# Kernel optimization log

Measured on AMD Instinct MI355X. Metric: run time of the kernel, lower is better.

Reference implementation:

```python
import jax, jax.numpy as jnp
import numpy as np

N_NODES = 100000
N_EDGES = 1600000
D_IN = 64
D_HID = 64


def setup_inputs() -> dict:
    key = jax.random.key(0)
    k1, k2, k3, k4, k5 = jax.random.split(key, 5)
    x = jax.random.normal(k1, (N_NODES, D_IN), dtype=jnp.float32)
    edge_index = jax.random.randint(k2, (2, N_EDGES), 0, N_NODES, dtype=jnp.int64)
    edge_weight = jax.random.uniform(k3, (N_EDGES,), dtype=jnp.float32)
    # GCNConv glorot-initialized linear weights (bias=False)
    s0 = (6.0 / (D_IN + D_HID)) ** 0.5
    W0 = jax.random.uniform(k4, (D_IN, D_HID), minval=-s0, maxval=s0, dtype=jnp.float32)
    s1 = (6.0 / (D_HID + D_HID)) ** 0.5
    W1 = jax.random.uniform(k5, (D_HID, D_HID), minval=-s1, maxval=s1, dtype=jnp.float32)
    return {"x": x, "edge_index": edge_index, "edge_weight": edge_weight, "W0": W0, "W1": W1}


def _gcn_layer(x, W, src, dst, edge_weight, deg_inv_sqrt, n_nodes):
    # h = X W  (bias=False)
    h = x @ W  # [N, D]
    # symmetric normalization including self-loops (weight 1)
    norm = deg_inv_sqrt[src] * edge_weight * deg_inv_sqrt[dst]  # [E]
    # gather src features, scale, scatter-sum at dst
    agg = jax.ops.segment_sum(norm[:, None] * h[src], dst, num_segments=n_nodes)
    # self-loop contribution: norm_ii = deg_inv_sqrt[i]^2 * 1
    agg = agg + (deg_inv_sqrt * deg_inv_sqrt)[:, None] * h
    return jax.nn.relu(agg)  # dropout is identity in eval mode


def reference(x, edge_index, edge_weight, W0, W1):
    src, dst = edge_index[0], edge_index[1]
    # degree with self-loops (self-loop weight = 1), aggregated at dst (source_to_target flow)
    deg = jax.ops.segment_sum(edge_weight, dst, num_segments=N_NODES) + 1.0
    deg_inv_sqrt = jax.lax.rsqrt(deg)
    x = _gcn_layer(x, W0, src, dst, edge_weight, deg_inv_sqrt, N_NODES)
    x = _gcn_layer(x, W1, src, dst, edge_weight, deg_inv_sqrt, N_NODES)
    return x
```

## Files before the change

### kernel.cpp

```cpp
#include <hip/hip_runtime.h>
#include <hip/hip_fp16.h>

#define D 64
#define BSH 9
#define BSZ (1 << BSH)
#define PB 2048
#define CAP 15360
#define SCAP 9216

__global__ __launch_bounds__(256) void initcur(int* __restrict__ ccur, int nbuck) {
    int t = threadIdx.x;
    if (t < nbuck) ccur[t] = t * CAP;
}

__global__ __launch_bounds__(512) void bucket1(const int* __restrict__ src,
                                               const int* __restrict__ dst,
                                               const float* __restrict__ ew,
                                               int* __restrict__ ccur,
                                               int2* __restrict__ pairs,
                                               int E, int nbuck) {
    __shared__ int hist[512];
    __shared__ int lbase[512];
    __shared__ int gbase[512];
    __shared__ int w0s[PB];
    __shared__ int w1s[PB];
    __shared__ unsigned short bids[PB];
    int t = threadIdx.x;
    hist[t] = 0;
    __syncthreads();
    int e0 = blockIdx.x * PB;
    int cnt = min(PB, E - e0);
    int b[4], lr[4], w0[4], w1[4];
    int i4 = t * 4;
    bool full4 = (i4 + 4 <= cnt);
    if (full4) {
        int4   s4 = *(const int4*)&src[e0 + i4];
        int4   d4 = *(const int4*)&dst[e0 + i4];
        float4 w4 = *(const float4*)&ew[e0 + i4];
        int ss[4] = {s4.x, s4.y, s4.z, s4.w};
        int ds[4] = {d4.x, d4.y, d4.z, d4.w};
        float wv[4] = {w4.x, w4.y, w4.z, w4.w};
#pragma unroll
        for (int k = 0; k < 4; ++k) {
            b[k]  = ds[k] >> BSH;
            w0[k] = ss[k] | ((ds[k] & (BSZ - 1)) << 17);
            w1[k] = __float_as_int(wv[k]);
            lr[k] = atomicAdd(&hist[b[k]], 1);
        }
    } else {
#pragma unroll
        for (int k = 0; k < 4; ++k) {
            int idx = i4 + k;
            if (idx < cnt) {
                int d = dst[e0 + idx];
                b[k]  = d >> BSH;
                w0[k] = src[e0 + idx] | ((d & (BSZ - 1)) << 17);
                w1[k] = __float_as_int(ew[e0 + idx]);
                lr[k] = atomicAdd(&hist[b[k]], 1);
            }
        }
    }
    __syncthreads();
    int hv = hist[t];
    lbase[t] = hv;
    __syncthreads();
    for (int off = 1; off < 512; off <<= 1) {
        int u = (t >= off) ? lbase[t - off] : 0;
        __syncthreads();
        lbase[t] += u;
        __syncthreads();
    }
    int excl = lbase[t] - hv;
    __syncthreads();
    lbase[t] = excl;
    if (t < nbuck && hv > 0) gbase[t] = atomicAdd(&ccur[t], hv);
    __syncthreads();
#pragma unroll
    for (int k = 0; k < 4; ++k) {
        int idx = i4 + k;
        if (idx < cnt) {
            int slot = lbase[b[k]] + lr[k];
            w0s[slot] = w0[k];
            w1s[slot] = w1[k];
            bids[slot] = (unsigned short)b[k];
        }
    }
    __syncthreads();
    for (int i = t; i < cnt; i += 512) {
        int bb = bids[i];
        int pos = gbase[bb] + (i - lbase[bb]);
        pairs[pos] = make_int2(w0s[i], w1s[i]);
    }
}

__global__ __launch_bounds__(512) void deg2(const int2* __restrict__ pairs,
                                            const int* __restrict__ ccur,
                                            int* __restrict__ offsets,
                                            int* __restrict__ ends,
                                            float* __restrict__ dis,
                                            int N, int nbuck) {
    __shared__ int cnt[512];
    __shared__ float sdeg[512];
    __shared__ int lb[512];
    int b = blockIdx.x;
    int t = threadIdx.x;
    cnt[t] = 0;
    sdeg[t] = 0.0f;
    __syncthreads();
    int base = b * CAP;
    int cntb = ccur[b] - base;
    for (int i = t; i < cntb; i += 512) {
        int2 p = pairs[base + i];
        int dl = p.x >> 17;
        atomicAdd(&cnt[dl], 1);
        atomicAdd(&sdeg[dl], __int_as_float(p.y));
    }
    __syncthreads();
    int node = (b << BSH) + t;
    int pc = (node < N) ? ((cnt[t] + 1 + 15) & ~15) : 0;
    lb[t] = pc;
    __syncthreads();
    for (int off = 1; off < 512; off <<= 1) {
        int u = (t >= off) ? lb[t - off] : 0;
        __syncthreads();
        lb[t] += u;
        __syncthreads();
    }
    int excl = lb[t] - pc;
    if (node < N) {
        offsets[node] = base + excl;
        ends[node]    = base + excl + pc;
        dis[node]     = rsqrtf(sdeg[t] + 1.0f);
    }
}

__global__ __launch_bounds__(512) void sort2b(int2* __restrict__ pairs,
                                              const int* __restrict__ ccur,
                                              const int* __restrict__ offsets,
                                              const int* __restrict__ ends,
                                              const float* __restrict__ dis,
                                              int N, int nbuck) {
    __shared__ int2 se[SCAP];
    __shared__ int cur[512];
    __shared__ float sdis[512];
    int b = blockIdx.x;
    int t = threadIdx.x;
    int base = b * CAP;
    int cntb = min(ccur[b] - base, SCAP);
    for (int i = t; i < cntb; i += 512) se[i] = pairs[base + i];
    int node = (b << BSH) + t;
    int end = 0; float dloc = 0.0f;
    if (node < N) {
        cur[t]  = offsets[node];
        end     = ends[node];
        dloc    = dis[node];
        sdis[t] = dloc;
    } else {
        cur[t] = 0; sdis[t] = 0.0f;
    }
    __syncthreads();
    for (int i = t; i < cntb; i += 512) {
        int2 p = se[i];
        int dl = p.x >> 17;
        int s  = p.x & 0x1FFFF;
        int pos = atomicAdd(&cur[dl], 1);
        float w = __int_as_float(p.y) * sdis[dl] * dis[s];
        pairs[pos] = make_int2(s, __float_as_int(w));
    }
    __syncthreads();
    if (node < N) {
        int c = cur[t];
        pairs[c] = make_int2(node, __float_as_int(dloc * dloc));
        for (int i = c + 1; i < end; ++i) pairs[i] = make_int2(0, 0);
    }
}

__global__ __launch_bounds__(256) void gemm64h(const float* __restrict__ X,
                                               const float* __restrict__ W,
                                               __half* __restrict__ Hb, int n) {
    __shared__ float Ws[64 * 64];
    __shared__ float Xs[16 * 64];
    for (int t = threadIdx.x; t < 64 * 64; t += 256) Ws[t] = W[t];
    int row0 = blockIdx.x * 16;
    for (int t = threadIdx.x; t < 16 * 64; t += 256) {
        int r = row0 + (t >> 6);
        Xs[t] = (r < n) ? X[r * 64 + (t & 63)] : 0.0f;
    }
    __syncthreads();
    int r  = threadIdx.x >> 4;
    int jc = (threadIdx.x & 15) * 4;
    float4 acc = make_float4(0.f, 0.f, 0.f, 0.f);
#pragma unroll
    for (int k = 0; k < 64; ++k) {
        float xv = Xs[r * 64 + k];
        float4 w = *(const float4*)&Ws[k * 64 + jc];
        acc.x += xv * w.x; acc.y += xv * w.y; acc.z += xv * w.z; acc.w += xv * w.w;
    }
    int rr = row0 + r;
    if (rr < n) {
        ushort4 pk;
        pk.x = __half_as_ushort(__float2half(acc.x));
        pk.y = __half_as_ushort(__float2half(acc.y));
        pk.z = __half_as_ushort(__float2half(acc.z));
        pk.w = __half_as_ushort(__float2half(acc.w));
        *(ushort4*)&Hb[rr * 64 + jc] = pk;
    }
}

__global__ __launch_bounds__(256) void gather64(const int2* __restrict__ pairs,
                                                const int* __restrict__ offsets,
                                                const int* __restrict__ ends,
                                                const __half* __restrict__ Hb,
                                                float* __restrict__ OUT, int N) {
    int node = blockIdx.x * 4 + (threadIdx.x >> 6);
    if (node >= N) return;
    int lane = threadIdx.x & 63;
    int g    = lane >> 3;
    int fl   = (lane & 7) * 8;
    int beg = offsets[node];
    int end = ends[node];
    __half2 z = __float2half2_rn(0.0f);
    __half2 a0[4] = {z, z, z, z};
    __half2 a1[4] = {z, z, z, z};
    for (int e = beg; e < end; e += 16) {
        int2 p0 = pairs[e + g];
        int2 p1 = pairs[e + 8 + g];
        __half2 w0 = __half2half2(__float2half(__int_as_float(p0.y)));
        __half2 w1 = __half2half2(__float2half(__int_as_float(p1.y)));
        uint4 r0 = *(const uint4*)(Hb + (size_t)p0.x * 64 + fl);
        uint4 r1 = *(const uint4*)(Hb + (size_t)p1.x * 64 + fl);
        const __half2* h0 = (const __half2*)&r0;
        const __half2* h1 = (const __half2*)&r1;
#pragma unroll
        for (int k = 0; k < 4; ++k) {
            a0[k] = __hfma2(w0, h0[k], a0[k]);
            a1[k] = __hfma2(w1, h1[k], a1[k]);
        }
    }
    __half2 a[4];
#pragma unroll
    for (int k = 0; k < 4; ++k) a[k] = __hadd2(a0[k], a1[k]);
#pragma unroll
    for (int m = 8; m < 64; m <<= 1) {
#pragma unroll
        for (int k = 0; k < 4; ++k) {
            unsigned u = __shfl_xor(*(unsigned*)&a[k], m, 64);
            a[k] = __hadd2(a[k], *(__half2*)&u);
        }
    }
    if (g < 2) {
        int o = g * 2;
        float2 f0 = __half22float2(a[o]);
        float2 f1 = __half22float2(a[o + 1]);
        float4 vv;
        vv.x = fmaxf(f0.x, 0.0f);
        vv.y = fmaxf(f0.y, 0.0f);
        vv.z = fmaxf(f1.x, 0.0f);
        vv.w = fmaxf(f1.y, 0.0f);
        *(float4*)&OUT[node * 64 + fl + g * 4] = vv;
    }
}

extern "C" void kernel_launch(void* const* d_in, const int* in_sizes, int n_in,
                              void* d_out, int out_size, void* d_ws, size_t ws_size,
                              hipStream_t stream) {
    const float* x  = (const float*)d_in[0];
    const int*   ei = (const int*)d_in[1];
    const float* ew = (const float*)d_in[2];
    const float* W0 = (const float*)d_in[3];
    const float* W1 = (const float*)d_in[4];
    float* out = (float*)d_out;

    const int N = in_sizes[0] / D;
    const int E = in_sizes[2];
    const int* src = ei;
    const int* dst = ei + E;

    const int nbuck = (N + BSZ - 1) >> BSH;
    const int Na = (N + 1 + 255) & ~255;

    float* dis     = (float*)d_ws;
    int*   offsets = (int*)d_ws + Na;
    int*   ends    = (int*)d_ws + 2 * Na;
    int*   ccur    = (int*)d_ws + 3 * Na;
    int2*  pairs   = (int2*)((int*)d_ws + 3 * Na + 1024);
    __half* Hb     = (__half*)(pairs + (size_t)nbuck * CAP);

    const int nb1 = (E + PB - 1) / PB;

    initcur<<<1, 256, 0, stream>>>(ccur, nbuck);
    bucket1<<<nb1, 512, 0, stream>>>(src, dst, ew, ccur, pairs, E, nbuck);
    deg2<<<nbuck, 512, 0, stream>>>(pairs, ccur, offsets, ends, dis, N, nbuck);
    sort2b<<<nbuck, 512, 0, stream>>>(pairs, ccur, offsets, ends, dis, N, nbuck);

    const int gemm_grid   = (N + 15) / 16;
    const int gather_grid = (N + 3) / 4;

    gemm64h<<<gemm_grid, 256, 0, stream>>>(x, W0, Hb, N);
    gather64<<<gather_grid, 256, 0, stream>>>(pairs, offsets, ends, Hb, out, N);

    gemm64h<<<gemm_grid, 256, 0, stream>>>(out, W1, Hb, N);
    gather64<<<gather_grid, 256, 0, stream>>>(pairs, offsets, ends, Hb, out, N);
}
```

Before: 217.1 us.

## Fuse degree and sort kernels, fold source normalization into GEMM, unroll gather

Merges the degree/offset kernel and the sort kernel into one pass that stages each bucket's pairs in shared memory once. The source-side rsqrt(deg) factor moves from the per-edge weight into the GEMM epilogue, which scales each row of H. This removes the random dis[s] lookups during sorting. The gather loop is unrolled to 32 edges per iteration with four accumulators to keep more loads in flight, and per-node padding grows from multiples of 16 to multiples of 32 (with CAP raised to match). In exchange, edges with more padding mean more zero entries in short lists, and fp16 rounding now applies to the prescaled H.

```diff
diff --git a/kernel.cpp b/kernel.cpp
--- a/kernel.cpp
+++ b/kernel.cpp
@@ -5,7 +5,7 @@
 #define BSH 9
 #define BSZ (1 << BSH)
 #define PB 2048
-#define CAP 15360
+#define CAP 18432
 #define SCAP 9216
 
 __global__ __launch_bounds__(256) void initcur(int* __restrict__ ccur, int nbuck) {
@@ -93,31 +93,34 @@
     }
 }
 
-__global__ __launch_bounds__(512) void deg2(const int2* __restrict__ pairs,
-                                            const int* __restrict__ ccur,
-                                            int* __restrict__ offsets,
-                                            int* __restrict__ ends,
-                                            float* __restrict__ dis,
-                                            int N, int nbuck) {
+__global__ __launch_bounds__(512) void sort2(int2* __restrict__ pairs,
+                                             const int* __restrict__ ccur,
+                                             int* __restrict__ offsets,
+                                             int* __restrict__ ends,
+                                             float* __restrict__ dis,
+                                             int N, int nbuck) {
+    __shared__ int2 se[SCAP];
     __shared__ int cnt[512];
     __shared__ float sdeg[512];
     __shared__ int lb[512];
+    __shared__ int cur[512];
     int b = blockIdx.x;
     int t = threadIdx.x;
+    int base = b * CAP;
+    int cntb = min(ccur[b] - base, SCAP);
+    for (int i = t; i < cntb; i += 512) se[i] = pairs[base + i];
     cnt[t] = 0;
     sdeg[t] = 0.0f;
     __syncthreads();
-    int base = b * CAP;
-    int cntb = ccur[b] - base;
     for (int i = t; i < cntb; i += 512) {
-        int2 p = pairs[base + i];
+        int2 p = se[i];
         int dl = p.x >> 17;
         atomicAdd(&cnt[dl], 1);
         atomicAdd(&sdeg[dl], __int_as_float(p.y));
     }
     __syncthreads();
     int node = (b << BSH) + t;
-    int pc = (node < N) ? ((cnt[t] + 1 + 15) & ~15) : 0;
+    int pc = (node < N) ? ((cnt[t] + 1 + 31) & ~31) : 0;
     lb[t] = pc;
     __syncthreads();
     for (int off = 1; off < 512; off <<= 1) {
@@ -127,36 +130,15 @@
         __syncthreads();
     }
     int excl = lb[t] - pc;
+    float dloc = rsqrtf(sdeg[t] + 1.0f);
+    __syncthreads();
+    sdeg[t] = dloc;
+    cur[t]  = base + excl;
+    int myend = base + excl + pc;
     if (node < N) {
         offsets[node] = base + excl;
-        ends[node]    = base + excl + pc;
-        dis[node]     = rsqrtf(sdeg[t] + 1.0f);
-    }
-}
-
-__global__ __launch_bounds__(512) void sort2b(int2* __restrict__ pairs,
-                                              const int* __restrict__ ccur,
-                                              const int* __restrict__ offsets,
-                                              const int* __restrict__ ends,
-                                              const float* __restrict__ dis,
-                                              int N, int nbuck) {
-    __shared__ int2 se[SCAP];
-    __shared__ int cur[512];
-    __shared__ float sdis[512];
-    int b = blockIdx.x;
-    int t = threadIdx.x;
-    int base = b * CAP;
-    int cntb = min(ccur[b] - base, SCAP);
-    for (int i = t; i < cntb; i += 512) se[i] = pairs[base + i];
-    int node = (b << BSH) + t;
-    int end = 0; float dloc = 0.0f;
-    if (node < N) {
-        cur[t]  = offsets[node];
-        end     = ends[node];
-        dloc    = dis[node];
-        sdis[t] = dloc;
-    } else {
-        cur[t] = 0; sdis[t] = 0.0f;
+        ends[node]    = myend;
+        dis[node]     = dloc;
     }
     __syncthreads();
     for (int i = t; i < cntb; i += 512) {
@@ -164,19 +146,20 @@
         int dl = p.x >> 17;
         int s  = p.x & 0x1FFFF;
         int pos = atomicAdd(&cur[dl], 1);
-        float w = __int_as_float(p.y) * sdis[dl] * dis[s];
+        float w = __int_as_float(p.y) * sdeg[dl];
         pairs[pos] = make_int2(s, __float_as_int(w));
     }
     __syncthreads();
     if (node < N) {
         int c = cur[t];
-        pairs[c] = make_int2(node, __float_as_int(dloc * dloc));
-        for (int i = c + 1; i < end; ++i) pairs[i] = make_int2(0, 0);
+        pairs[c] = make_int2(node, __float_as_int(dloc));
+        for (int i = c + 1; i < myend; ++i) pairs[i] = make_int2(0, 0);
     }
 }
 
 __global__ __launch_bounds__(256) void gemm64h(const float* __restrict__ X,
                                                const float* __restrict__ W,
+                                               const float* __restrict__ dis,
                                                __half* __restrict__ Hb, int n) {
     __shared__ float Ws[64 * 64];
     __shared__ float Xs[16 * 64];
@@ -198,11 +181,12 @@
     }
     int rr = row0 + r;
     if (rr < n) {
+        float ds = dis[rr];
         ushort4 pk;
-        pk.x = __half_as_ushort(__float2half(acc.x));
-        pk.y = __half_as_ushort(__float2half(acc.y));
-        pk.z = __half_as_ushort(__float2half(acc.z));
-        pk.w = __half_as_ushort(__float2half(acc.w));
+        pk.x = __half_as_ushort(__float2half(ds * acc.x));
+        pk.y = __half_as_ushort(__float2half(ds * acc.y));
+        pk.z = __half_as_ushort(__float2half(ds * acc.z));
+        pk.w = __half_as_ushort(__float2half(ds * acc.w));
         *(ushort4*)&Hb[rr * 64 + jc] = pk;
     }
 }
@@ -222,24 +206,37 @@
     __half2 z = __float2half2_rn(0.0f);
     __half2 a0[4] = {z, z, z, z};
     __half2 a1[4] = {z, z, z, z};
-    for (int e = beg; e < end; e += 16) {
+    __half2 a2[4] = {z, z, z, z};
+    __half2 a3[4] = {z, z, z, z};
+    for (int e = beg; e < end; e += 32) {
         int2 p0 = pairs[e + g];
         int2 p1 = pairs[e + 8 + g];
+        int2 p2 = pairs[e + 16 + g];
+        int2 p3 = pairs[e + 24 + g];
+        uint4 r0 = *(const uint4*)(Hb + (size_t)p0.x * 64 + fl);
+        uint4 r1 = *(const uint4*)(Hb + (size_t)p1.x * 64 + fl);
+        uint4 r2 = *(const uint4*)(Hb + (size_t)p2.x * 64 + fl);
+        uint4 r3 = *(const uint4*)(Hb + (size_t)p3.x * 64 + fl);
         __half2 w0 = __half2half2(__float2half(__int_as_float(p0.y)));
         __half2 w1 = __half2half2(__float2half(__int_as_float(p1.y)));
-        uint4 r0 = *(const uint4*)(Hb + (size_t)p0.x * 64 + fl);
-        uint4 r1 = *(const uint4*)(Hb + (size_t)p1.x * 64 + fl);
+        __half2 w2 = __half2half2(__float2half(__int_as_float(p2.y)));
+        __half2 w3 = __half2half2(__float2half(__int_as_float(p3.y)));
         const __half2* h0 = (const __half2*)&r0;
         const __half2* h1 = (const __half2*)&r1;
+        const __half2* h2 = (const __half2*)&r2;
+        const __half2* h3 = (const __half2*)&r3;
 #pragma unroll
         for (int k = 0; k < 4; ++k) {
             a0[k] = __hfma2(w0, h0[k], a0[k]);
             a1[k] = __hfma2(w1, h1[k], a1[k]);
+            a2[k] = __hfma2(w2, h2[k], a2[k]);
+            a3[k] = __hfma2(w3, h3[k], a3[k]);
         }
     }
     __half2 a[4];
 #pragma unroll
-    for (int k = 0; k < 4; ++k) a[k] = __hadd2(a0[k], a1[k]);
+    for (int k = 0; k < 4; ++k)
+        a[k] = __hadd2(__hadd2(a0[k], a1[k]), __hadd2(a2[k], a3[k]));
 #pragma unroll
     for (int m = 8; m < 64; m <<= 1) {
 #pragma unroll
@@ -290,15 +287,14 @@
 
     initcur<<<1, 256, 0, stream>>>(ccur, nbuck);
     bucket1<<<nb1, 512, 0, stream>>>(src, dst, ew, ccur, pairs, E, nbuck);
-    deg2<<<nbuck, 512, 0, stream>>>(pairs, ccur, offsets, ends, dis, N, nbuck);
-    sort2b<<<nbuck, 512, 0, stream>>>(pairs, ccur, offsets, ends, dis, N, nbuck);
+    sort2<<<nbuck, 512, 0, stream>>>(pairs, ccur, offsets, ends, dis, N, nbuck);
 
     const int gemm_grid   = (N + 15) / 16;
     const int gather_grid = (N + 3) / 4;
 
-    gemm64h<<<gemm_grid, 256, 0, stream>>>(x, W0, Hb, N);
+    gemm64h<<<gemm_grid, 256, 0, stream>>>(x, W0, dis, Hb, N);
     gather64<<<gather_grid, 256, 0, stream>>>(pairs, offsets, ends, Hb, out, N);
 
-    gemm64h<<<gemm_grid, 256, 0, stream>>>(out, W1, Hb, N);
+    gemm64h<<<gemm_grid, 256, 0, stream>>>(out, W1, dis, Hb, N);
     gather64<<<gather_grid, 256, 0, stream>>>(pairs, offsets, ends, Hb, out, N);
 }
```

After: 212.1 us. -2.3%, faster.
